# Performance work log

Measured on AMD Instinct MI355X. Metric: run time of the kernel, lower is better.

## Reference

```python
import jax, jax.numpy as jnp
import numpy as np

N, E, F, H, C = 50000, 800000, 128, 128, 64
NEG_SLOPE = 0.2


def setup_inputs() -> dict:
    key = jax.random.key(0)
    ks = jax.random.split(key, 12)
    s = 1.0 / np.sqrt(H)
    return {
        "x": jax.random.normal(ks[0], (N, F), jnp.float32),
        "edge_index": jax.random.randint(ks[1], (2, E), 0, N, jnp.int64),
        "W1": jax.random.normal(ks[2], (F, H), jnp.float32) * s,
        "b1": jnp.zeros((H,), jnp.float32),
        "Wg1": jax.random.normal(ks[3], (H, H), jnp.float32) * s,
        "asrc1": jax.random.normal(ks[4], (H,), jnp.float32) * s,
        "adst1": jax.random.normal(ks[5], (H,), jnp.float32) * s,
        "bg1": jnp.zeros((H,), jnp.float32),
        "W2": jax.random.normal(ks[6], (H, H), jnp.float32) * s,
        "b2": jnp.zeros((H,), jnp.float32),
        "Wg2": jax.random.normal(ks[7], (H, H), jnp.float32) * s,
        "asrc2": jax.random.normal(ks[8], (H,), jnp.float32) * s,
        "adst2": jax.random.normal(ks[9], (H,), jnp.float32) * s,
        "bg2": jnp.zeros((H,), jnp.float32),
        "Wo": jax.random.normal(ks[10], (H, C), jnp.float32) * s,
        "bo": jnp.zeros((C,), jnp.float32),
    }


def _gcn(x, src, dst, n, W, b):
    # PyG GCNConv: add self-loops (done by caller), symmetric normalization
    xw = x @ W
    deg = jax.ops.segment_sum(jnp.ones(src.shape[0], xw.dtype), dst, num_segments=n)
    inv = jax.lax.rsqrt(deg)  # deg >= 1 due to self-loops
    coef = inv[src] * inv[dst]
    return jax.ops.segment_sum(coef[:, None] * xw[src], dst, num_segments=n) + b


def _gat(x, src, dst, n, W, a_s, a_d, b):
    # PyG GATConv, heads=1: segment softmax over destination nodes
    xw = x @ W
    e = jax.nn.leaky_relu((xw @ a_s)[src] + (xw @ a_d)[dst], NEG_SLOPE)
    m = jax.ops.segment_max(e, dst, num_segments=n)
    ex = jnp.exp(e - m[dst])
    denom = jax.ops.segment_sum(ex, dst, num_segments=n)
    alpha = ex / denom[dst]
    return jax.ops.segment_sum(alpha[:, None] * xw[src], dst, num_segments=n) + b


def reference(x, edge_index, W1, b1, Wg1, asrc1, adst1, bg1,
              W2, b2, Wg2, asrc2, adst2, bg2, Wo, bo):
    n = x.shape[0]
    loops = jnp.arange(n, dtype=edge_index.dtype)
    src = jnp.concatenate([edge_index[0], loops])
    dst = jnp.concatenate([edge_index[1], loops])

    h = jax.nn.relu(_gcn(x, src, dst, n, W1, b1))
    h = jax.nn.relu(_gat(h, src, dst, n, Wg1, asrc1, adst1, bg1))
    h = jax.nn.relu(_gcn(h, src, dst, n, W2, b2))
    h = jax.nn.relu(_gat(h, src, dst, n, Wg2, asrc2, adst2, bg2))
    z = h @ Wo + bo
    return (h, z)
```

## Files before the change

kernel.cpp:

```cpp
#include <hip/hip_runtime.h>
#include <hip/hip_bf16.h>
#include <hip/hip_fp16.h>


#define WAVE 64
#define BK 256
#define CHUNK 4096

typedef _Float16 f16x8 __attribute__((ext_vector_type(8)));
typedef float f32x4 __attribute__((ext_vector_type(4)));

__global__ void k_zero_i32(int* __restrict__ p, int n) {
    int i = blockIdx.x * 256 + threadIdx.x;
    if (i < n) p[i] = 0;
}


__global__ __launch_bounds__(256) void k_bhist(
    const int* __restrict__ ei, int* __restrict__ bcnt,
    int E, int Et, int nbuck) {
    __shared__ int hist[256];
    int tid = threadIdx.x;
    if (tid < nbuck) hist[tid] = 0;
    __syncthreads();
    for (int e = blockIdx.x * 256 + tid; e < Et; e += gridDim.x * 256) {
        int d = (e < E) ? ei[E + e] : (e - E);
        atomicAdd(&hist[d >> 8], 1);
    }
    __syncthreads();
    if (tid < nbuck && hist[tid] > 0) atomicAdd(&bcnt[tid], hist[tid]);
}

__global__ void k_bscan(const int* __restrict__ bcnt, int* __restrict__ bbase,
                        int* __restrict__ bcur, int nbuck) {
    __shared__ int tmp[256];
    int tid = threadIdx.x;
    int v = (tid < nbuck) ? bcnt[tid] : 0;
    tmp[tid] = v;
    __syncthreads();
    for (int off = 1; off < 256; off <<= 1) {
        int t = (tid >= off) ? tmp[tid - off] : 0;
        __syncthreads();
        tmp[tid] += t;
        __syncthreads();
    }
    if (tid < nbuck) {
        int excl = tmp[tid] - v;
        bbase[tid] = excl;
        bcur[tid] = excl;
        if (tid == nbuck - 1) bbase[nbuck] = tmp[tid];
    }
}

__global__ __launch_bounds__(256) void k_bscatter(
    const int* __restrict__ ei, int* __restrict__ bcur,
    int2* __restrict__ ebuf, int E, int Et, int nbuck) {
    __shared__ int hist[256];
    __shared__ int base[256];
    __shared__ int off[256];
    constexpr int PT = CHUNK / 256;
    int tid = threadIdx.x;
    int cb = blockIdx.x * CHUNK;
    if (tid < nbuck) { hist[tid] = 0; off[tid] = 0; }
    __syncthreads();

    int sv[PT], dv[PT];
#pragma unroll
    for (int i = 0; i < PT; ++i) {
        int e = cb + i * 256 + tid;
        int s = 0, d = -1;
        if (e < Et) {
            if (e < E) { s = ei[e]; d = ei[E + e]; }
            else       { s = d = e - E; }
            atomicAdd(&hist[d >> 8], 1);
        }
        sv[i] = s; dv[i] = d;
    }
    __syncthreads();
    if (tid < nbuck && hist[tid] > 0)
        base[tid] = atomicAdd(&bcur[tid], hist[tid]);
    __syncthreads();
#pragma unroll
    for (int i = 0; i < PT; ++i) {
        if (dv[i] >= 0) {
            int b = dv[i] >> 8;
            int pos = base[b] + atomicAdd(&off[b], 1);
            ebuf[pos] = make_int2(sv[i], dv[i]);
        }
    }
}

__global__ __launch_bounds__(256) void k_csr(
    const int2* __restrict__ ebuf, const int* __restrict__ bbase,
    int* __restrict__ rowp, float* __restrict__ inv, int* __restrict__ esrc,
    int Nn, int Et) {
    __shared__ int hist[256];
    __shared__ int scan[256];
    __shared__ int cur[256];
    int tid = threadIdx.x;
    int b = blockIdx.x;
    int bb = bbase[b], cnt = bbase[b + 1] - bb;
    hist[tid] = 0;
    __syncthreads();
    for (int t = tid; t < cnt; t += 256)
        atomicAdd(&hist[ebuf[bb + t].y & 255], 1);
    __syncthreads();
    int v = hist[tid];
    scan[tid] = v;
    __syncthreads();
    for (int o = 1; o < 256; o <<= 1) {
        int t = (tid >= o) ? scan[tid - o] : 0;
        __syncthreads();
        scan[tid] += t;
        __syncthreads();
    }
    int excl = scan[tid] - v;
    int node = b * BK + tid;
    if (node < Nn) {
        rowp[node] = bb + excl;
        inv[node] = rsqrtf((float)v);
    }
    cur[tid] = excl;
    if (b == 0 && tid == 0) rowp[Nn] = Et;
    __syncthreads();
    for (int t = tid; t < cnt; t += 256) {
        int2 e = ebuf[bb + t];
        int pos = bb + atomicAdd(&cur[e.y & 255], 1);
        esrc[pos] = e.x;
    }
}


__global__ void k_wcvt(const float* __restrict__ W1, const float* __restrict__ Wg1,
                       const float* __restrict__ W2, const float* __restrict__ Wg2,
                       const float* __restrict__ Wo, __half* __restrict__ Wt) {
    int i = blockIdx.x * 256 + threadIdx.x;
    if (i < 65536) {
        int w = i >> 14;
        int j = i & 16383;
        int n = j >> 7, k = j & 127;
        const float* W = (w == 0) ? W1 : (w == 1) ? Wg1 : (w == 2) ? W2 : Wg2;
        Wt[i] = __float2half(W[k * 128 + n]);
    } else if (i < 73728) {
        int j = i - 65536;
        int n = j >> 7, k = j & 127;
        Wt[65536 + j] = __float2half(Wo[k * 64 + n]);
    }
}


template <int NC, typename OT>
__global__ __launch_bounds__(256) void gemm_mfma(
    const float* __restrict__ A, const __half* __restrict__ Wt,
    const float* __restrict__ bias, OT* __restrict__ out,
    const float* __restrict__ asrc, const float* __restrict__ adst,
    float* __restrict__ alS, float* __restrict__ alD, int M) {
    constexpr int NT = NC / 16;
    constexpr int LDW = 136;
    __shared__ _Float16 Wl[NC * LDW];
    const int tid = threadIdx.x;
    const int wv = tid >> 6, lane = tid & 63;
    const int m16 = lane & 15, quad = lane >> 4;

    for (int i = tid; i < NC * 16; i += 256) {
        int r = i >> 4, c8 = i & 15;
        *(float4*)(&Wl[r * LDW + c8 * 8]) =
            *(const float4*)((const _Float16*)Wt + r * 128 + c8 * 8);
    }
    __syncthreads();

    const int row0 = blockIdx.x * 128 + wv * 32;

    f16x8 af[2][4];
#pragma unroll
    for (int mt = 0; mt < 2; ++mt) {
        int row = row0 + mt * 16 + m16;
        if (row > M - 1) row = M - 1;
        const float* ap = A + (size_t)row * 128 + quad * 8;
#pragma unroll
        for (int ks = 0; ks < 4; ++ks) {
            float4 lo = *(const float4*)(ap + ks * 32);
            float4 hi = *(const float4*)(ap + ks * 32 + 4);
            f16x8 v;
            v[0] = (_Float16)lo.x; v[1] = (_Float16)lo.y;
            v[2] = (_Float16)lo.z; v[3] = (_Float16)lo.w;
            v[4] = (_Float16)hi.x; v[5] = (_Float16)hi.y;
            v[6] = (_Float16)hi.z; v[7] = (_Float16)hi.w;
            af[mt][ks] = v;
        }
    }

    f32x4 acc[2][NT];
#pragma unroll
    for (int mt = 0; mt < 2; ++mt)
#pragma unroll
        for (int nt = 0; nt < NT; ++nt)
            acc[mt][nt] = (f32x4){0.f, 0.f, 0.f, 0.f};

#pragma unroll
    for (int ks = 0; ks < 4; ++ks) {
#pragma unroll
        for (int nt = 0; nt < NT; ++nt) {
            f16x8 bf = *(const f16x8*)(&Wl[(nt * 16 + m16) * LDW + ks * 32 + quad * 8]);
            acc[0][nt] = __builtin_amdgcn_mfma_f32_16x16x32_f16(
                af[0][ks], bf, acc[0][nt], 0, 0, 0);
            acc[1][nt] = __builtin_amdgcn_mfma_f32_16x16x32_f16(
                af[1][ks], bf, acc[1][nt], 0, 0, 0);
        }
    }

    if (asrc) {
        float sa[NT], da[NT];
#pragma unroll
        for (int nt = 0; nt < NT; ++nt) {
            sa[nt] = asrc[nt * 16 + m16];
            da[nt] = adst[nt * 16 + m16];
        }
#pragma unroll
        for (int mt = 0; mt < 2; ++mt) {
#pragma unroll
            for (int r = 0; r < 4; ++r) {
                float s = 0.f, d = 0.f;
#pragma unroll
                for (int nt = 0; nt < NT; ++nt) {
                    s = fmaf(acc[mt][nt][r], sa[nt], s);
                    d = fmaf(acc[mt][nt][r], da[nt], d);
                }
#pragma unroll
                for (int off = 8; off > 0; off >>= 1) {
                    s += __shfl_xor(s, off);
                    d += __shfl_xor(d, off);
                }
                int row = row0 + mt * 16 + quad * 4 + r;
                if (m16 == 0 && row < M) { alS[row] = s; alD[row] = d; }
            }
        }
    }

#pragma unroll
    for (int mt = 0; mt < 2; ++mt) {
#pragma unroll
        for (int nt = 0; nt < NT; ++nt) {
#pragma unroll
            for (int r = 0; r < 4; ++r) {
                int row = row0 + mt * 16 + quad * 4 + r;
                if (row < M) {
                    float v = acc[mt][nt][r];
                    int col = nt * 16 + m16;
                    if constexpr (sizeof(OT) == 2) {
                        ((__half*)out)[(size_t)row * NC + col] = __float2half(v);
                    } else {
                        ((float*)out)[(size_t)row * NC + col] = v + bias[col];
                    }
                }
            }
        }
    }
}


__device__ __forceinline__ void gather_accum_h(
    const __half* __restrict__ xw, int q, int g, int cnt, int sid, float wgt,
    float acc[8]) {
    for (int base = 0; base < cnt; base += 32) {
        int c = cnt - base;
        float4 x[8];
        float w[8];
#pragma unroll
        for (int u = 0; u < 8; ++u) {
            if (u * 4 < c) {
                int idx = base + 4 * u + g;
                int s = __shfl(sid, idx);
                w[u] = __shfl(wgt, idx);
                x[u] = *(const float4*)(xw + (size_t)s * 128 + q * 8);
            }
        }
#pragma unroll
        for (int u = 0; u < 8; ++u) {
            if (u * 4 < c) {
                const __half2* h2 = (const __half2*)&x[u];
#pragma unroll
                for (int i = 0; i < 4; ++i) {
                    float2 cc = __half22float2(h2[i]);
                    acc[2 * i]     = fmaf(w[u], cc.x, acc[2 * i]);
                    acc[2 * i + 1] = fmaf(w[u], cc.y, acc[2 * i + 1]);
                }
            }
        }
    }
}

__device__ __forceinline__ void finish_store_q(
    float acc[8], const float* __restrict__ bias, float* __restrict__ out,
    int n, int q, int g) {
#pragma unroll
    for (int i = 0; i < 8; ++i) {
        acc[i] += __shfl_xor(acc[i], 16);
        acc[i] += __shfl_xor(acc[i], 32);
    }
    if (g == 0) {
        float4 b0 = ((const float4*)bias)[q * 2];
        float4 b1 = ((const float4*)bias)[q * 2 + 1];
        float4 r0, r1;
        r0.x = fmaxf(acc[0] + b0.x, 0.f);
        r0.y = fmaxf(acc[1] + b0.y, 0.f);
        r0.z = fmaxf(acc[2] + b0.z, 0.f);
        r0.w = fmaxf(acc[3] + b0.w, 0.f);
        r1.x = fmaxf(acc[4] + b1.x, 0.f);
        r1.y = fmaxf(acc[5] + b1.y, 0.f);
        r1.z = fmaxf(acc[6] + b1.z, 0.f);
        r1.w = fmaxf(acc[7] + b1.w, 0.f);
        float4* orow = (float4*)(out + (size_t)n * 128);
        orow[q * 2]     = r0;
        orow[q * 2 + 1] = r1;
    }
}

__global__ __launch_bounds__(256) void k_gcn_agg(
    const __half* __restrict__ xw, const int* __restrict__ rowp,
    const int* __restrict__ esrc, const float* __restrict__ inv,
    const float* __restrict__ bias, float* __restrict__ out, int Nn) {
    int gid = blockIdx.x * 256 + threadIdx.x;
    int n = gid >> 6, lane = gid & 63;
    if (n >= Nn) return;
    int q = lane & 15, g = lane >> 4;
    int beg = rowp[n], end = rowp[n + 1];
    float invd = inv[n];
    float acc[8] = {0.f, 0.f, 0.f, 0.f, 0.f, 0.f, 0.f, 0.f};
    for (int base = beg; base < end; base += WAVE) {
        int e = base + lane;
        bool valid = (e < end);
        int sid = valid ? esrc[e] : 0;
        float c = valid ? invd * inv[sid] : 0.f;
        gather_accum_h(xw, q, g, min(WAVE, end - base), sid, c, acc);
    }
    finish_store_q(acc, bias, out, n, q, g);
}

__global__ __launch_bounds__(256) void k_gat_agg(
    const __half* __restrict__ xw, const int* __restrict__ rowp,
    const int* __restrict__ esrc, const float* __restrict__ as_,
    const float* __restrict__ ad_, const float* __restrict__ bias,
    float* __restrict__ out, int Nn) {
    int gid = blockIdx.x * 256 + threadIdx.x;
    int n = gid >> 6, lane = gid & 63;
    if (n >= Nn) return;
    int q = lane & 15, g = lane >> 4;
    int beg = rowp[n], end = rowp[n + 1];
    int deg = end - beg;
    float adn = ad_[n];
    float acc[8] = {0.f, 0.f, 0.f, 0.f, 0.f, 0.f, 0.f, 0.f};

    if (deg <= WAVE) {
        bool valid = (lane < deg);
        int sid = 0;
        float v = -1e30f;
        if (valid) {
            sid = esrc[beg + lane];
            float t = as_[sid] + adn;
            v = (t > 0.f) ? t : 0.2f * t;
        }
        float m = v;
#pragma unroll
        for (int off = 32; off > 0; off >>= 1) m = fmaxf(m, __shfl_xor(m, off));
        float ex = valid ? __expf(v - m) : 0.f;
        float ssum = ex;
#pragma unroll
        for (int off = 32; off > 0; off >>= 1) ssum += __shfl_xor(ssum, off);
        float wgt = ex * (1.f / ssum);
        gather_accum_h(xw, q, g, deg, sid, wgt, acc);
    } else {
        float m = -1e30f, ssum = 0.f;
        for (int e = beg + lane; e < end; e += WAVE) {
            float v = as_[esrc[e]] + adn;
            v = (v > 0.f) ? v : 0.2f * v;
            float mn = fmaxf(m, v);
            ssum = ssum * __expf(m - mn) + __expf(v - mn);
            m = mn;
        }
#pragma unroll
        for (int off = 32; off > 0; off >>= 1) {
            float mo = __shfl_xor(m, off);
            float so = __shfl_xor(ssum, off);
            float mn = fmaxf(m, mo);
            ssum = ssum * __expf(m - mn) + so * __expf(mo - mn);
            m = mn;
        }
        float rden = 1.f / ssum;
        for (int base = beg; base < end; base += WAVE) {
            int e = base + lane;
            bool valid = (e < end);
            int sid = valid ? esrc[e] : 0;
            float wgt = 0.f;
            if (valid) {
                float v = as_[sid] + adn;
                v = (v > 0.f) ? v : 0.2f * v;
                wgt = __expf(v - m) * rden;
            }
            gather_accum_h(xw, q, g, min(WAVE, end - base), sid, wgt, acc);
        }
    }
    finish_store_q(acc, bias, out, n, q, g);
}


extern "C" void kernel_launch(void* const* d_in, const int* in_sizes, int n_in,
                              void* d_out, int out_size, void* d_ws, size_t ws_size,
                              hipStream_t stream) {
    const float* x   = (const float*)d_in[0];
    const int*   ei  = (const int*)d_in[1];
    const float* W1  = (const float*)d_in[2];
    const float* b1  = (const float*)d_in[3];
    const float* Wg1 = (const float*)d_in[4];
    const float* as1 = (const float*)d_in[5];
    const float* ad1 = (const float*)d_in[6];
    const float* bg1 = (const float*)d_in[7];
    const float* W2  = (const float*)d_in[8];
    const float* b2  = (const float*)d_in[9];
    const float* Wg2 = (const float*)d_in[10];
    const float* as2 = (const float*)d_in[11];
    const float* ad2 = (const float*)d_in[12];
    const float* bg2 = (const float*)d_in[13];
    const float* Wo  = (const float*)d_in[14];
    const float* bo  = (const float*)d_in[15];

    const int Nn = in_sizes[0] / 128;
    const int E  = in_sizes[1] / 2;
    const int Et = E + Nn;
    const int H  = 128;
    const int nbuck = (Nn + BK - 1) / BK;

    float* outH = (float*)d_out;
    float* outZ = outH + (size_t)Nn * H;

    char* p = (char*)d_ws;
    auto carve = [&](size_t bytes) {
        char* r = p;
        p += (bytes + 255) & ~(size_t)255;
        return r;
    };
    __half* bufA = (__half*)carve((size_t)Nn * H * sizeof(__half));
    __half* Wt   = (__half*)carve((size_t)73728 * sizeof(__half));
    float* alS   = (float*)carve((size_t)Nn * sizeof(float));
    float* alD   = (float*)carve((size_t)Nn * sizeof(float));
    float* inv   = (float*)carve((size_t)Nn * sizeof(float));
    int*   rowp  = (int*)carve((size_t)(Nn + 1) * sizeof(int));
    int*   esrc  = (int*)carve((size_t)Et * sizeof(int));
    int2*  ebuf  = (int2*)carve((size_t)Et * sizeof(int2));
    int*   bcnt  = (int*)carve((size_t)nbuck * sizeof(int));
    int*   bbase = (int*)carve((size_t)(nbuck + 1) * sizeof(int));
    int*   bcur  = (int*)carve((size_t)nbuck * sizeof(int));
    (void)ws_size; (void)n_in; (void)out_size;

    const int aggBlocks = (Nn * WAVE + 255) / 256;
    const int gemmB = (Nn + 127) / 128;
    const int scatB = (Et + CHUNK - 1) / CHUNK;

    k_zero_i32<<<1, 256, 0, stream>>>(bcnt, nbuck);
    k_bhist<<<104, 256, 0, stream>>>(ei, bcnt, E, Et, nbuck);
    k_bscan<<<1, 256, 0, stream>>>(bcnt, bbase, bcur, nbuck);
    k_bscatter<<<scatB, 256, 0, stream>>>(ei, bcur, ebuf, E, Et, nbuck);
    k_csr<<<nbuck, 256, 0, stream>>>(ebuf, bbase, rowp, inv, esrc, Nn, Et);
    k_wcvt<<<288, 256, 0, stream>>>(W1, Wg1, W2, Wg2, Wo, Wt);

    gemm_mfma<128, __half><<<gemmB, 256, 0, stream>>>(
        x, Wt, nullptr, bufA, nullptr, nullptr, nullptr, nullptr, Nn);
    k_gcn_agg<<<aggBlocks, 256, 0, stream>>>(bufA, rowp, esrc, inv, b1, outH, Nn);

    gemm_mfma<128, __half><<<gemmB, 256, 0, stream>>>(
        outH, Wt + 16384, nullptr, bufA, as1, ad1, alS, alD, Nn);
    k_gat_agg<<<aggBlocks, 256, 0, stream>>>(bufA, rowp, esrc, alS, alD, bg1, outH, Nn);

    gemm_mfma<128, __half><<<gemmB, 256, 0, stream>>>(
        outH, Wt + 32768, nullptr, bufA, nullptr, nullptr, nullptr, nullptr, Nn);
    k_gcn_agg<<<aggBlocks, 256, 0, stream>>>(bufA, rowp, esrc, inv, b2, outH, Nn);

    gemm_mfma<128, __half><<<gemmB, 256, 0, stream>>>(
        outH, Wt + 49152, nullptr, bufA, as2, ad2, alS, alD, Nn);
    k_gat_agg<<<aggBlocks, 256, 0, stream>>>(bufA, rowp, esrc, alS, alD, bg2, outH, Nn);

    gemm_mfma<64, float><<<gemmB, 256, 0, stream>>>(
        outH, Wt + 65536, bo, outZ, nullptr, nullptr, nullptr, nullptr, Nn);
}
```

Before: 381.4 us.

## Precompute per-edge weights and split gather into column-slice blocks

Edge weights (GCN normalisation and GAT softmax) are now computed in separate kernels and stored per edge, reusing the freed edge buffer. The GCN weights are computed once and shared by both GCN layers. The gather kernel is split across four 32-column slices so that each wave reads 64-byte row segments for 16 edges at a time instead of full 256-byte rows. The split is meant to raise parallelism and improve cache locality per slice. In exchange it adds extra launches and reads the CSR indices and weights four times.

```diff
diff --git a/kernel.cpp b/kernel.cpp
--- a/kernel.cpp
+++ b/kernel.cpp
@@ -259,48 +259,127 @@
 }
 
 
-__device__ __forceinline__ void gather_accum_h(
-    const __half* __restrict__ xw, int q, int g, int cnt, int sid, float wgt,
-    float acc[8]) {
-    for (int base = 0; base < cnt; base += 32) {
-        int c = cnt - base;
-        float4 x[8];
-        float w[8];
-#pragma unroll
-        for (int u = 0; u < 8; ++u) {
-            if (u * 4 < c) {
-                int idx = base + 4 * u + g;
-                int s = __shfl(sid, idx);
-                w[u] = __shfl(wgt, idx);
-                x[u] = *(const float4*)(xw + (size_t)s * 128 + q * 8);
+__global__ __launch_bounds__(256) void k_ewg(
+    const int* __restrict__ rowp, const int* __restrict__ esrc,
+    const float* __restrict__ inv, float* __restrict__ ew, int Nn) {
+    int gid = blockIdx.x * 256 + threadIdx.x;
+    int n = gid >> 6, lane = gid & 63;
+    if (n >= Nn) return;
+    int beg = rowp[n], end = rowp[n + 1];
+    float invd = inv[n];
+    for (int e = beg + lane; e < end; e += WAVE)
+        ew[e] = invd * inv[esrc[e]];
+}
+
+__global__ __launch_bounds__(256) void k_ewa(
+    const int* __restrict__ rowp, const int* __restrict__ esrc,
+    const float* __restrict__ alS, const float* __restrict__ alD,
+    float* __restrict__ ew, int Nn) {
+    int gid = blockIdx.x * 256 + threadIdx.x;
+    int n = gid >> 6, lane = gid & 63;
+    if (n >= Nn) return;
+    int beg = rowp[n], end = rowp[n + 1];
+    int deg = end - beg;
+    float adn = alD[n];
+
+    if (deg <= WAVE) {
+        bool vld = (lane < deg);
+        float v = -1e30f;
+        if (vld) {
+            float t = alS[esrc[beg + lane]] + adn;
+            v = (t > 0.f) ? t : 0.2f * t;
+        }
+        float m = v;
+#pragma unroll
+        for (int off = 32; off > 0; off >>= 1) m = fmaxf(m, __shfl_xor(m, off));
+        float ex = vld ? __expf(v - m) : 0.f;
+        float ssum = ex;
+#pragma unroll
+        for (int off = 32; off > 0; off >>= 1) ssum += __shfl_xor(ssum, off);
+        if (vld) ew[beg + lane] = ex * (1.f / ssum);
+    } else {
+        float m = -1e30f, ssum = 0.f;
+        for (int e = beg + lane; e < end; e += WAVE) {
+            float v = alS[esrc[e]] + adn;
+            v = (v > 0.f) ? v : 0.2f * v;
+            float mn = fmaxf(m, v);
+            ssum = ssum * __expf(m - mn) + __expf(v - mn);
+            m = mn;
+        }
+#pragma unroll
+        for (int off = 32; off > 0; off >>= 1) {
+            float mo = __shfl_xor(m, off);
+            float so = __shfl_xor(ssum, off);
+            float mn = fmaxf(m, mo);
+            ssum = ssum * __expf(m - mn) + so * __expf(mo - mn);
+            m = mn;
+        }
+        float rden = 1.f / ssum;
+        for (int e = beg + lane; e < end; e += WAVE) {
+            float v = alS[esrc[e]] + adn;
+            v = (v > 0.f) ? v : 0.2f * v;
+            ew[e] = __expf(v - m) * rden;
+        }
+    }
+}
+
+
+__global__ __launch_bounds__(256) void k_gather(
+    const __half* __restrict__ xw, const int* __restrict__ rowp,
+    const int* __restrict__ esrc, const float* __restrict__ ew,
+    const float* __restrict__ bias, float* __restrict__ out,
+    int Nn, int nodeBlk) {
+    int s = blockIdx.x / nodeBlk;
+    int nb = blockIdx.x - s * nodeBlk;
+    int wv = threadIdx.x >> 6, lane = threadIdx.x & 63;
+    int n = nb * 4 + wv;
+    if (n >= Nn) return;
+    int g = lane >> 2, cq = lane & 3;
+    int beg = rowp[n], end = rowp[n + 1];
+    const __half* xs = xw + s * 32 + cq * 8;
+
+    float acc[8] = {0.f, 0.f, 0.f, 0.f, 0.f, 0.f, 0.f, 0.f};
+    for (int base = beg; base < end; base += WAVE) {
+        int c = end - base;
+        int e = base + lane;
+        bool vld = (e < end);
+        int sid = vld ? esrc[e] : 0;
+        float w = vld ? ew[e] : 0.f;
+        float4 x[4];
+        float wg[4];
+#pragma unroll
+        for (int r = 0; r < 4; ++r) {
+            if (r * 16 < c) {
+                int idx = r * 16 + g;
+                int sg = __shfl(sid, idx);
+                wg[r] = __shfl(w, idx);
+                x[r] = *(const float4*)(xs + (size_t)sg * 128);
             }
         }
 #pragma unroll
-        for (int u = 0; u < 8; ++u) {
-            if (u * 4 < c) {
-                const __half2* h2 = (const __half2*)&x[u];
+        for (int r = 0; r < 4; ++r) {
+            if (r * 16 < c) {
+                const __half2* h2 = (const __half2*)&x[r];
 #pragma unroll
                 for (int i = 0; i < 4; ++i) {
                     float2 cc = __half22float2(h2[i]);
-                    acc[2 * i]     = fmaf(w[u], cc.x, acc[2 * i]);
-                    acc[2 * i + 1] = fmaf(w[u], cc.y, acc[2 * i + 1]);
+                    acc[2 * i]     = fmaf(wg[r], cc.x, acc[2 * i]);
+                    acc[2 * i + 1] = fmaf(wg[r], cc.y, acc[2 * i + 1]);
                 }
             }
         }
     }
-}
-
-__device__ __forceinline__ void finish_store_q(
-    float acc[8], const float* __restrict__ bias, float* __restrict__ out,
-    int n, int q, int g) {
 #pragma unroll
     for (int i = 0; i < 8; ++i) {
+        acc[i] += __shfl_xor(acc[i], 4);
+        acc[i] += __shfl_xor(acc[i], 8);
         acc[i] += __shfl_xor(acc[i], 16);
         acc[i] += __shfl_xor(acc[i], 32);
     }
     if (g == 0) {
-        float4 b0 = ((const float4*)bias)[q * 2];
-        float4 b1 = ((const float4*)bias)[q * 2 + 1];
+        int col = s * 32 + cq * 8;
+        float4 b0 = *(const float4*)(bias + col);
+        float4 b1 = *(const float4*)(bias + col + 4);
         float4 r0, r1;
         r0.x = fmaxf(acc[0] + b0.x, 0.f);
         r0.y = fmaxf(acc[1] + b0.y, 0.f);
@@ -310,97 +389,9 @@
         r1.y = fmaxf(acc[5] + b1.y, 0.f);
         r1.z = fmaxf(acc[6] + b1.z, 0.f);
         r1.w = fmaxf(acc[7] + b1.w, 0.f);
-        float4* orow = (float4*)(out + (size_t)n * 128);
-        orow[q * 2]     = r0;
-        orow[q * 2 + 1] = r1;
-    }
-}
-
-__global__ __launch_bounds__(256) void k_gcn_agg(
-    const __half* __restrict__ xw, const int* __restrict__ rowp,
-    const int* __restrict__ esrc, const float* __restrict__ inv,
-    const float* __restrict__ bias, float* __restrict__ out, int Nn) {
-    int gid = blockIdx.x * 256 + threadIdx.x;
-    int n = gid >> 6, lane = gid & 63;
-    if (n >= Nn) return;
-    int q = lane & 15, g = lane >> 4;
-    int beg = rowp[n], end = rowp[n + 1];
-    float invd = inv[n];
-    float acc[8] = {0.f, 0.f, 0.f, 0.f, 0.f, 0.f, 0.f, 0.f};
-    for (int base = beg; base < end; base += WAVE) {
-        int e = base + lane;
-        bool valid = (e < end);
-        int sid = valid ? esrc[e] : 0;
-        float c = valid ? invd * inv[sid] : 0.f;
-        gather_accum_h(xw, q, g, min(WAVE, end - base), sid, c, acc);
-    }
-    finish_store_q(acc, bias, out, n, q, g);
-}
-
-__global__ __launch_bounds__(256) void k_gat_agg(
-    const __half* __restrict__ xw, const int* __restrict__ rowp,
-    const int* __restrict__ esrc, const float* __restrict__ as_,
-    const float* __restrict__ ad_, const float* __restrict__ bias,
-    float* __restrict__ out, int Nn) {
-    int gid = blockIdx.x * 256 + threadIdx.x;
-    int n = gid >> 6, lane = gid & 63;
-    if (n >= Nn) return;
-    int q = lane & 15, g = lane >> 4;
-    int beg = rowp[n], end = rowp[n + 1];
-    int deg = end - beg;
-    float adn = ad_[n];
-    float acc[8] = {0.f, 0.f, 0.f, 0.f, 0.f, 0.f, 0.f, 0.f};
-
-    if (deg <= WAVE) {
-        bool valid = (lane < deg);
-        int sid = 0;
-        float v = -1e30f;
-        if (valid) {
-            sid = esrc[beg + lane];
-            float t = as_[sid] + adn;
-            v = (t > 0.f) ? t : 0.2f * t;
-        }
-        float m = v;
-#pragma unroll
-        for (int off = 32; off > 0; off >>= 1) m = fmaxf(m, __shfl_xor(m, off));
-        float ex = valid ? __expf(v - m) : 0.f;
-        float ssum = ex;
-#pragma unroll
-        for (int off = 32; off > 0; off >>= 1) ssum += __shfl_xor(ssum, off);
-        float wgt = ex * (1.f / ssum);
-        gather_accum_h(xw, q, g, deg, sid, wgt, acc);
-    } else {
-        float m = -1e30f, ssum = 0.f;
-        for (int e = beg + lane; e < end; e += WAVE) {
-            float v = as_[esrc[e]] + adn;
-            v = (v > 0.f) ? v : 0.2f * v;
-            float mn = fmaxf(m, v);
-            ssum = ssum * __expf(m - mn) + __expf(v - mn);
-            m = mn;
-        }
-#pragma unroll
-        for (int off = 32; off > 0; off >>= 1) {
-            float mo = __shfl_xor(m, off);
-            float so = __shfl_xor(ssum, off);
-            float mn = fmaxf(m, mo);
-            ssum = ssum * __expf(m - mn) + so * __expf(mo - mn);
-            m = mn;
-        }
-        float rden = 1.f / ssum;
-        for (int base = beg; base < end; base += WAVE) {
-            int e = base + lane;
-            bool valid = (e < end);
-            int sid = valid ? esrc[e] : 0;
-            float wgt = 0.f;
-            if (valid) {
-                float v = as_[sid] + adn;
-                v = (v > 0.f) ? v : 0.2f * v;
-                wgt = __expf(v - m) * rden;
-            }
-            gather_accum_h(xw, q, g, min(WAVE, end - base), sid, wgt, acc);
-        }
-    }
-    finish_store_q(acc, bias, out, n, q, g);
+        *(float4*)(out + (size_t)n * 128 + col)     = r0;
+        *(float4*)(out + (size_t)n * 128 + col + 4) = r1;
+    }
 }
 
 
@@ -450,11 +441,15 @@
     int*   bcnt  = (int*)carve((size_t)nbuck * sizeof(int));
     int*   bbase = (int*)carve((size_t)(nbuck + 1) * sizeof(int));
     int*   bcur  = (int*)carve((size_t)nbuck * sizeof(int));
+    float* ewG = (float*)ebuf;
+    float* ewA = (float*)ebuf + Et;
     (void)ws_size; (void)n_in; (void)out_size;
 
-    const int aggBlocks = (Nn * WAVE + 255) / 256;
-    const int gemmB = (Nn + 127) / 128;
-    const int scatB = (Et + CHUNK - 1) / CHUNK;
+    const int nodeW  = (Nn * WAVE + 255) / 256;
+    const int gemmB  = (Nn + 127) / 128;
+    const int scatB  = (Et + CHUNK - 1) / CHUNK;
+    const int nodeBlk = (Nn + 3) / 4;
+    const int gathB  = 4 * nodeBlk;
 
     k_zero_i32<<<1, 256, 0, stream>>>(bcnt, nbuck);
     k_bhist<<<104, 256, 0, stream>>>(ei, bcnt, E, Et, nbuck);
@@ -462,22 +457,25 @@
     k_bscatter<<<scatB, 256, 0, stream>>>(ei, bcur, ebuf, E, Et, nbuck);
     k_csr<<<nbuck, 256, 0, stream>>>(ebuf, bbase, rowp, inv, esrc, Nn, Et);
     k_wcvt<<<288, 256, 0, stream>>>(W1, Wg1, W2, Wg2, Wo, Wt);
+    k_ewg<<<nodeW, 256, 0, stream>>>(rowp, esrc, inv, ewG, Nn);
 
     gemm_mfma<128, __half><<<gemmB, 256, 0, stream>>>(
         x, Wt, nullptr, bufA, nullptr, nullptr, nullptr, nullptr, Nn);
-    k_gcn_agg<<<aggBlocks, 256, 0, stream>>>(bufA, rowp, esrc, inv, b1, outH, Nn);
+    k_gather<<<gathB, 256, 0, stream>>>(bufA, rowp, esrc, ewG, b1, outH, Nn, nodeBlk);
 
     gemm_mfma<128, __half><<<gemmB, 256, 0, stream>>>(
         outH, Wt + 16384, nullptr, bufA, as1, ad1, alS, alD, Nn);
-    k_gat_agg<<<aggBlocks, 256, 0, stream>>>(bufA, rowp, esrc, alS, alD, bg1, outH, Nn);
+    k_ewa<<<nodeW, 256, 0, stream>>>(rowp, esrc, alS, alD, ewA, Nn);
+    k_gather<<<gathB, 256, 0, stream>>>(bufA, rowp, esrc, ewA, bg1, outH, Nn, nodeBlk);
 
     gemm_mfma<128, __half><<<gemmB, 256, 0, stream>>>(
         outH, Wt + 32768, nullptr, bufA, nullptr, nullptr, nullptr, nullptr, Nn);
-    k_gcn_agg<<<aggBlocks, 256, 0, stream>>>(bufA, rowp, esrc, inv, b2, outH, Nn);
+    k_gather<<<gathB, 256, 0, stream>>>(bufA, rowp, esrc, ewG, b2, outH, Nn, nodeBlk);
 
     gemm_mfma<128, __half><<<gemmB, 256, 0, stream>>>(
         outH, Wt + 49152, nullptr, bufA, as2, ad2, alS, alD, Nn);
-    k_gat_agg<<<aggBlocks, 256, 0, stream>>>(bufA, rowp, esrc, alS, alD, bg2, outH, Nn);
+    k_ewa<<<nodeW, 256, 0, stream>>>(rowp, esrc, alS, alD, ewA, Nn);
+    k_gather<<<gathB, 256, 0, stream>>>(bufA, rowp, esrc, ewA, bg2, outH, Nn, nodeBlk);
 
     gemm_mfma<64, float><<<gemmB, 256, 0, stream>>>(
         outH, Wt + 65536, bo, outZ, nullptr, nullptr, nullptr, nullptr, Nn);
```

New measurement: 565.7 us. +48.3%, slower.
